# Optimization experiments

Measured on AMD Instinct MI355X. Metric: run time of the kernel, lower is better.

Reference implementation:

```python
import jax, jax.numpy as jnp
import numpy as np


def _piecewise_weights(gt):
    # stats over gt[0,0]; torch.std uses ddof=1
    g00 = gt[0, 0]
    gmin = jnp.min(g00)
    gmean = jnp.mean(g00)
    gmax = jnp.max(g00)
    sd = jnp.std(g00, ddof=1)
    m1 = gmean + sd
    m2 = gmean + 3.0 * sd
    w_low = (gt - gmin) / (m1 - gmin) * 0.2
    w_mid = (gt - m1) / (m2 - m1) * 0.5 + 0.2
    w_high = (gt - m2) / (gmax - m2) * 0.3 + 0.7
    return jnp.where(gt <= m1, w_low, jnp.where(gt <= m2, w_mid, w_high))


def setup_inputs() -> dict:
    key = jax.random.key(0)
    k1, k2 = jax.random.split(key)
    shape = (1, 1, 4096, 4096)
    inputs = jax.random.normal(k1, shape, dtype=jnp.float32)
    targets = jax.random.normal(k2, shape, dtype=jnp.float32)
    return {"inputs": inputs, "targets": targets}


def reference(inputs, targets):
    # gt is a detached clone of targets -> no grad through the weights
    gt = jax.lax.stop_gradient(targets)
    weights = _piecewise_weights(gt)
    loss = jnp.abs(targets - inputs)
    return jnp.mean(loss * weights)
```

## Files before the change

### kernel.cpp

```cpp
#include <hip/hip_runtime.h>
#include <math.h>

#define BS 256
#define NB 2048
#define NWAVES (BS / 64)
#define TBS 1024
#define TNW (TBS / 64)

__device__ inline double wred_sum(double v) {
#pragma unroll
    for (int o = 32; o > 0; o >>= 1) v += __shfl_down(v, o, 64);
    return v;
}
__device__ inline float wred_min(float v) {
#pragma unroll
    for (int o = 32; o > 0; o >>= 1) v = fminf(v, __shfl_down(v, o, 64));
    return v;
}
__device__ inline float wred_max(float v) {
#pragma unroll
    for (int o = 32; o > 0; o >>= 1) v = fmaxf(v, __shfl_down(v, o, 64));
    return v;
}

__device__ inline void acc_stats(float4 v, double& s, double& ss, float& mn, float& mx) {
    mn = fminf(mn, fminf(fminf(v.x, v.y), fminf(v.z, v.w)));
    mx = fmaxf(mx, fmaxf(fmaxf(v.x, v.y), fmaxf(v.z, v.w)));
    s += (double)v.x + (double)v.y + (double)v.z + (double)v.w;
    ss += (double)v.x * v.x + (double)v.y * v.y
        + (double)v.z * v.z + (double)v.w * v.w;
}

__global__ void __launch_bounds__(BS) k_stats(
        const float* __restrict__ t, int n,
        double* __restrict__ bsum, double* __restrict__ bss,
        float* __restrict__ bmn, float* __restrict__ bmx) {
    int tid = blockIdx.x * BS + threadIdx.x;
    const int stride = NB * BS;
    int n4 = n >> 2;
    const float4* t4 = (const float4*)t;

    double s = 0.0, ss = 0.0;
    float mn = 3.4e38f, mx = -3.4e38f;
    int i = tid;
    for (; i + 3 * stride < n4; i += 4 * stride) {
        float4 a = t4[i];
        float4 b = t4[i + stride];
        float4 c = t4[i + 2 * stride];
        float4 d = t4[i + 3 * stride];
        acc_stats(a, s, ss, mn, mx);
        acc_stats(b, s, ss, mn, mx);
        acc_stats(c, s, ss, mn, mx);
        acc_stats(d, s, ss, mn, mx);
    }
    for (; i < n4; i += stride) {
        float4 a = t4[i];
        acc_stats(a, s, ss, mn, mx);
    }
    if (tid == 0) {
        for (int j = (n4 << 2); j < n; j++) {
            float v = t[j];
            mn = fminf(mn, v); mx = fmaxf(mx, v);
            s += v; ss += (double)v * v;
        }
    }

    s = wred_sum(s); ss = wred_sum(ss); mn = wred_min(mn); mx = wred_max(mx);

    __shared__ double sh_s[NWAVES], sh_ss[NWAVES];
    __shared__ float sh_mn[NWAVES], sh_mx[NWAVES];
    int wid = threadIdx.x >> 6, lane = threadIdx.x & 63;
    if (lane == 0) { sh_s[wid] = s; sh_ss[wid] = ss; sh_mn[wid] = mn; sh_mx[wid] = mx; }
    __syncthreads();
    if (threadIdx.x == 0) {
        double S = sh_s[0], SS = sh_ss[0];
        float MN = sh_mn[0], MX = sh_mx[0];
        for (int k = 1; k < NWAVES; k++) {
            S += sh_s[k]; SS += sh_ss[k];
            MN = fminf(MN, sh_mn[k]); MX = fmaxf(MX, sh_mx[k]);
        }
        bsum[blockIdx.x] = S; bss[blockIdx.x] = SS;
        bmn[blockIdx.x] = MN; bmx[blockIdx.x] = MX;
    }
}

__global__ void __launch_bounds__(TBS) k_finalize_stats(
        const double* __restrict__ bsum, const double* __restrict__ bss,
        const float* __restrict__ bmn, const float* __restrict__ bmx,
        long long n, float* __restrict__ stats) {
    double s = 0.0, ss = 0.0;
    float mn = 3.4e38f, mx = -3.4e38f;
    for (int i = threadIdx.x; i < NB; i += TBS) {
        s += bsum[i]; ss += bss[i];
        mn = fminf(mn, bmn[i]); mx = fmaxf(mx, bmx[i]);
    }
    s = wred_sum(s); ss = wred_sum(ss); mn = wred_min(mn); mx = wred_max(mx);

    __shared__ double sh_s[TNW], sh_ss[TNW];
    __shared__ float sh_mn[TNW], sh_mx[TNW];
    int wid = threadIdx.x >> 6, lane = threadIdx.x & 63;
    if (lane == 0) { sh_s[wid] = s; sh_ss[wid] = ss; sh_mn[wid] = mn; sh_mx[wid] = mx; }
    __syncthreads();
    if (threadIdx.x == 0) {
        double S = sh_s[0], SS = sh_ss[0];
        float MN = sh_mn[0], MX = sh_mx[0];
        for (int i = 1; i < TNW; i++) {
            S += sh_s[i]; SS += sh_ss[i];
            MN = fminf(MN, sh_mn[i]); MX = fmaxf(MX, sh_mx[i]);
        }
        double dn = (double)n;
        double mean = S / dn;
        double var = (SS - S * S / dn) / (dn - 1.0);
        double sd = sqrt(var);
        float gmin = MN, gmax = MX;
        float m1 = (float)(mean + sd);
        float m2 = (float)(mean + 3.0 * sd);
        stats[0] = gmin;
        stats[1] = m1;
        stats[2] = m2;
        stats[3] = gmax;
        stats[4] = 0.2f / (m1 - gmin);
        stats[5] = 0.5f / (m2 - m1);
        stats[6] = 0.3f / (gmax - m2);
    }
}

__device__ inline float welem(float g, float x, float gmin, float m1, float m2,
                              float sl, float sm, float shv) {
    float w = (g <= m1) ? (g - gmin) * sl
            : (g <= m2) ? (g - m1) * sm + 0.2f
                        : (g - m2) * shv + 0.7f;
    return fabsf(g - x) * w;
}

__device__ inline float wquad(float4 tv, float4 xv, float gmin, float m1,
                              float m2, float sl, float sm, float shv) {
    return welem(tv.x, xv.x, gmin, m1, m2, sl, sm, shv)
         + welem(tv.y, xv.y, gmin, m1, m2, sl, sm, shv)
         + welem(tv.z, xv.z, gmin, m1, m2, sl, sm, shv)
         + welem(tv.w, xv.w, gmin, m1, m2, sl, sm, shv);
}

__global__ void __launch_bounds__(BS) k_loss(
        const float* __restrict__ x, const float* __restrict__ t, int n,
        const float* __restrict__ stats, double* __restrict__ bsum) {
    float gmin = stats[0], m1 = stats[1], m2 = stats[2];
    float sl = stats[4], sm = stats[5], shv = stats[6];
    int tid = blockIdx.x * BS + threadIdx.x;
    const int stride = NB * BS;
    int n4 = n >> 2;
    const float4* x4 = (const float4*)x;
    const float4* t4 = (const float4*)t;

    int nfull = n4 / stride;
    int nmain = nfull & ~1;
    double acc = 0.0;

    if (nmain >= 2) {
        float4 ta = t4[tid],           xa = x4[tid];
        float4 tb = t4[tid + stride],  xb = x4[tid + stride];
        int i = tid + 2 * stride;
        for (int k = 2; k < nmain; k += 2, i += 2 * stride) {
            float4 tc = t4[i],          xc = x4[i];
            float4 td = t4[i + stride], xd = x4[i + stride];
            float e = wquad(ta, xa, gmin, m1, m2, sl, sm, shv);
            float f = wquad(tb, xb, gmin, m1, m2, sl, sm, shv);
            acc += (double)e + (double)f;
            ta = tc; xa = xc; tb = td; xb = xd;
        }
        float e = wquad(ta, xa, gmin, m1, m2, sl, sm, shv);
        float f = wquad(tb, xb, gmin, m1, m2, sl, sm, shv);
        acc += (double)e + (double)f;
    }
    for (int i = tid + nmain * stride; i < n4; i += stride) {
        float4 tv = t4[i], xv = x4[i];
        acc += (double)wquad(tv, xv, gmin, m1, m2, sl, sm, shv);
    }
    if (tid == 0) {
        for (int j = (n4 << 2); j < n; j++)
            acc += (double)welem(t[j], x[j], gmin, m1, m2, sl, sm, shv);
    }

    acc = wred_sum(acc);
    __shared__ double sh_s[NWAVES];
    int wid = threadIdx.x >> 6, lane = threadIdx.x & 63;
    if (lane == 0) sh_s[wid] = acc;
    __syncthreads();
    if (threadIdx.x == 0) {
        double S = sh_s[0];
        for (int k = 1; k < NWAVES; k++) S += sh_s[k];
        bsum[blockIdx.x] = S;
    }
}

__global__ void __launch_bounds__(TBS) k_final(
        const double* __restrict__ bsum, long long n, float* __restrict__ out) {
    double s = 0.0;
    for (int i = threadIdx.x; i < NB; i += TBS) s += bsum[i];
    s = wred_sum(s);
    __shared__ double sh_s[TNW];
    int wid = threadIdx.x >> 6, lane = threadIdx.x & 63;
    if (lane == 0) sh_s[wid] = s;
    __syncthreads();
    if (threadIdx.x == 0) {
        double S = sh_s[0];
        for (int i = 1; i < TNW; i++) S += sh_s[i];
        out[0] = (float)(S / (double)n);
    }
}

extern "C" void kernel_launch(void* const* d_in, const int* in_sizes, int n_in,
                              void* d_out, int out_size, void* d_ws, size_t ws_size,
                              hipStream_t stream) {
    const float* inp = (const float*)d_in[0];
    const float* tgt = (const float*)d_in[1];
    int n = in_sizes[0];

    char* ws = (char*)d_ws;
    double* sum1  = (double*)(ws);
    double* ss1   = (double*)(ws + 16384);
    float*  mn1   = (float*)(ws + 32768);
    float*  mx1   = (float*)(ws + 40960);
    float*  stats = (float*)(ws + 49152);
    double* sum2  = (double*)(ws + 49280);

    k_stats<<<NB, BS, 0, stream>>>(tgt, n, sum1, ss1, mn1, mx1);
    k_finalize_stats<<<1, TBS, 0, stream>>>(sum1, ss1, mn1, mx1, (long long)n, stats);
    k_loss<<<NB, BS, 0, stream>>>(inp, tgt, n, stats, sum2);
    k_final<<<1, TBS, 0, stream>>>(sum2, (long long)n, (float*)d_out);
}
```

Measured before the change: 45.49 us.

## Switch stats and loss kernels to contiguous per-block chunks with 4x unroll

Both the stats and loss kernels now give each block a contiguous chunk of the array instead of a grid-stride interleave. Inside the chunk each thread strides by the block size, with four float4 loads in flight per iteration. The loss kernel drops its software-pipelined double-buffer loop for a plain 4-way unrolled loop, and the piecewise weight is computed branch-free with fma before a select. The aim is better DRAM page and L2 locality, possibly with the targets chunk read by stats still cached when the loss kernel reads it, at the cost of losing explicit prefetch.

```diff
diff --git a/kernel.cpp b/kernel.cpp
--- a/kernel.cpp
+++ b/kernel.cpp
@@ -35,29 +35,30 @@
         const float* __restrict__ t, int n,
         double* __restrict__ bsum, double* __restrict__ bss,
         float* __restrict__ bmn, float* __restrict__ bmx) {
-    int tid = blockIdx.x * BS + threadIdx.x;
-    const int stride = NB * BS;
     int n4 = n >> 2;
+    int cpb = (n4 + NB - 1) / NB;
+    int start = blockIdx.x * cpb;
+    int end = min(start + cpb, n4);
     const float4* t4 = (const float4*)t;
 
     double s = 0.0, ss = 0.0;
     float mn = 3.4e38f, mx = -3.4e38f;
-    int i = tid;
-    for (; i + 3 * stride < n4; i += 4 * stride) {
+    int i = start + threadIdx.x;
+    for (; i + 3 * BS < end; i += 4 * BS) {
         float4 a = t4[i];
-        float4 b = t4[i + stride];
-        float4 c = t4[i + 2 * stride];
-        float4 d = t4[i + 3 * stride];
+        float4 b = t4[i + BS];
+        float4 c = t4[i + 2 * BS];
+        float4 d = t4[i + 3 * BS];
         acc_stats(a, s, ss, mn, mx);
         acc_stats(b, s, ss, mn, mx);
         acc_stats(c, s, ss, mn, mx);
         acc_stats(d, s, ss, mn, mx);
     }
-    for (; i < n4; i += stride) {
+    for (; i < end; i += BS) {
         float4 a = t4[i];
         acc_stats(a, s, ss, mn, mx);
     }
-    if (tid == 0) {
+    if (blockIdx.x == 0 && threadIdx.x == 0) {
         for (int j = (n4 << 2); j < n; j++) {
             float v = t[j];
             mn = fminf(mn, v); mx = fmaxf(mx, v);
@@ -127,10 +128,12 @@
 
 __device__ inline float welem(float g, float x, float gmin, float m1, float m2,
                               float sl, float sm, float shv) {
-    float w = (g <= m1) ? (g - gmin) * sl
-            : (g <= m2) ? (g - m1) * sm + 0.2f
-                        : (g - m2) * shv + 0.7f;
-    return fabsf(g - x) * w;
+    float d = fabsf(g - x);
+    float wlo = (g - gmin) * sl;
+    float wmi = fmaf(g - m1, sm, 0.2f);
+    float whi = fmaf(g - m2, shv, 0.7f);
+    float w = (g <= m1) ? wlo : ((g <= m2) ? wmi : whi);
+    return d * w;
 }
 
 __device__ inline float wquad(float4 tv, float4 xv, float gmin, float m1,
@@ -146,37 +149,31 @@
         const float* __restrict__ stats, double* __restrict__ bsum) {
     float gmin = stats[0], m1 = stats[1], m2 = stats[2];
     float sl = stats[4], sm = stats[5], shv = stats[6];
-    int tid = blockIdx.x * BS + threadIdx.x;
-    const int stride = NB * BS;
     int n4 = n >> 2;
+    int cpb = (n4 + NB - 1) / NB;
+    int start = blockIdx.x * cpb;
+    int end = min(start + cpb, n4);
     const float4* x4 = (const float4*)x;
     const float4* t4 = (const float4*)t;
 
-    int nfull = n4 / stride;
-    int nmain = nfull & ~1;
     double acc = 0.0;
-
-    if (nmain >= 2) {
-        float4 ta = t4[tid],           xa = x4[tid];
-        float4 tb = t4[tid + stride],  xb = x4[tid + stride];
-        int i = tid + 2 * stride;
-        for (int k = 2; k < nmain; k += 2, i += 2 * stride) {
-            float4 tc = t4[i],          xc = x4[i];
-            float4 td = t4[i + stride], xd = x4[i + stride];
-            float e = wquad(ta, xa, gmin, m1, m2, sl, sm, shv);
-            float f = wquad(tb, xb, gmin, m1, m2, sl, sm, shv);
-            acc += (double)e + (double)f;
-            ta = tc; xa = xc; tb = td; xb = xd;
-        }
-        float e = wquad(ta, xa, gmin, m1, m2, sl, sm, shv);
-        float f = wquad(tb, xb, gmin, m1, m2, sl, sm, shv);
-        acc += (double)e + (double)f;
-    }
-    for (int i = tid + nmain * stride; i < n4; i += stride) {
+    int i = start + threadIdx.x;
+    for (; i + 3 * BS < end; i += 4 * BS) {
+        float4 ta = t4[i];            float4 xa = x4[i];
+        float4 tb = t4[i + BS];       float4 xb = x4[i + BS];
+        float4 tc = t4[i + 2 * BS];   float4 xc = x4[i + 2 * BS];
+        float4 td = t4[i + 3 * BS];   float4 xd = x4[i + 3 * BS];
+        float e0 = wquad(ta, xa, gmin, m1, m2, sl, sm, shv);
+        float e1 = wquad(tb, xb, gmin, m1, m2, sl, sm, shv);
+        float e2 = wquad(tc, xc, gmin, m1, m2, sl, sm, shv);
+        float e3 = wquad(td, xd, gmin, m1, m2, sl, sm, shv);
+        acc += (double)(e0 + e1) + (double)(e2 + e3);
+    }
+    for (; i < end; i += BS) {
         float4 tv = t4[i], xv = x4[i];
         acc += (double)wquad(tv, xv, gmin, m1, m2, sl, sm, shv);
     }
-    if (tid == 0) {
+    if (blockIdx.x == 0 && threadIdx.x == 0) {
         for (int j = (n4 << 2); j < n; j++)
             acc += (double)welem(t[j], x[j], gmin, m1, m2, sl, sm, shv);
     }
```

New measurement: 44.11 us. 3.0% less time.
